# Kernel tuning notes

Measured on AMD Instinct MI355X. Metric: run time of the kernel, lower is better.

The kernel has to match this reference:

```python
import jax, jax.numpy as jnp
import numpy as np

N_NODES = 50000


def gat_layer(x, src, dst, W, att_s, att_d, b, concat):
    # PyG GATConv (eval mode): h = x W reshaped to [N, H, C]
    H, C = att_s.shape
    h = (x @ W).reshape(-1, H, C)                      # [N, H, C]
    a_s = (h * att_s).sum(-1)                          # [N, H]
    a_d = (h * att_d).sum(-1)                          # [N, H]
    e = jax.nn.leaky_relu(a_s[src] + a_d[dst], 0.2)    # [E, H]
    # scatter-softmax over destination nodes
    m = jax.ops.segment_max(e, dst, num_segments=N_NODES)
    alpha = jnp.exp(e - m[dst])
    denom = jax.ops.segment_sum(alpha, dst, num_segments=N_NODES)
    alpha = alpha / denom[dst]                         # [E, H]
    msg = h[src] * alpha[:, :, None]                   # [E, H, C]
    out = jax.ops.segment_sum(msg, dst, num_segments=N_NODES)  # [N, H, C]
    out = out.reshape(N_NODES, H * C) if concat else out.mean(axis=1)
    return out + b


def setup_inputs() -> dict:
    key = jax.random.key(0)
    ks = jax.random.split(key, 16)
    F_IN, HID, HEADS, NCLS, E = 512, 64, 4, 40, 800000
    x = jax.random.normal(ks[0], (N_NODES, F_IN), dtype=jnp.float32)
    edge_index = jax.random.randint(ks[1], (2, E), 0, N_NODES, dtype=jnp.int32)

    def glorot(k, shape):
        fan = shape[0]
        return jax.random.normal(k, shape, dtype=jnp.float32) / np.sqrt(fan)

    d1 = HID * HEADS  # 256
    return {
        "x": x,
        "edge_index": edge_index,
        "W1": glorot(ks[2], (F_IN, d1)),
        "as1": glorot(ks[3], (HEADS, HID)),
        "ad1": glorot(ks[4], (HEADS, HID)),
        "b1": jnp.zeros((d1,), jnp.float32),
        "W2": glorot(ks[5], (d1, d1)),
        "as2": glorot(ks[6], (HEADS, HID)),
        "ad2": glorot(ks[7], (HEADS, HID)),
        "b2": jnp.zeros((d1,), jnp.float32),
        "W3": glorot(ks[8], (d1, NCLS)),
        "as3": glorot(ks[9], (1, NCLS)),
        "ad3": glorot(ks[10], (1, NCLS)),
        "b3": jnp.zeros((NCLS,), jnp.float32),
    }


def reference(x, edge_index, W1, as1, ad1, b1, W2, as2, ad2, b2, W3, as3, ad3, b3):
    # add self-loops (PyG GATConv default)
    loops = jnp.arange(N_NODES, dtype=edge_index.dtype)
    src = jnp.concatenate([edge_index[0], loops])
    dst = jnp.concatenate([edge_index[1], loops])
    h = jax.nn.elu(gat_layer(x, src, dst, W1, as1, ad1, b1, True))
    h = jax.nn.elu(gat_layer(h, src, dst, W2, as2, ad2, b2, True))
    out = gat_layer(h, src, dst, W3, as3, ad3, b3, False)
    return out
```

## Files before the change

### kernel.cpp

```cpp
#include <hip/hip_runtime.h>
#include <stdint.h>

#define NN 50000
#define NB 196

typedef unsigned short u16;
typedef _Float16 f16;
typedef __attribute__((ext_vector_type(8))) _Float16 half8;
typedef __attribute__((ext_vector_type(4))) _Float16 half4;
typedef __attribute__((ext_vector_type(4))) float f32x4;

__device__ __forceinline__ void gload_lds16(const void* gsrc, void* ldst){
  __builtin_amdgcn_global_load_lds(
      (const __attribute__((address_space(1))) unsigned int*)gsrc,
      (__attribute__((address_space(3))) unsigned int*)ldst,
      16, 0, 0);
}

#define VMW(N)  asm volatile("s_waitcnt vmcnt(" #N ")" ::: "memory")
#define LGKM0() asm volatile("s_waitcnt lgkmcnt(0)" ::: "memory")
#define BARR()  asm volatile("s_barrier" ::: "memory")


__global__ void count_k(const int* __restrict__ dst, int* __restrict__ cnt, int E){
  int i = blockIdx.x * 256 + threadIdx.x;
  int tot = E + NN;
  if (i >= tot) return;
  int d = (i < E) ? dst[i] : (i - E);
  atomicAdd(&cnt[d], 1);
}

__global__ __launch_bounds__(256) void scan_part_k(const int* __restrict__ cnt,
                                                   int* __restrict__ bsum){
  __shared__ int lds[256];
  int tid = threadIdx.x;
  int idx = blockIdx.x * 256 + tid;
  lds[tid] = (idx < NN) ? cnt[idx] : 0;
  __syncthreads();
#pragma unroll
  for (int off = 128; off >= 1; off >>= 1){
    if (tid < off) lds[tid] += lds[tid + off];
    __syncthreads();
  }
  if (tid == 0) bsum[blockIdx.x] = lds[0];
}

__global__ __launch_bounds__(256) void scan_top_k(const int* __restrict__ bsum,
                                                  int* __restrict__ boff,
                                                  int* __restrict__ row_ptr){
  __shared__ int lds[256];
  int tid = threadIdx.x;
  int v = (tid < NB) ? bsum[tid] : 0;
  lds[tid] = v;
  __syncthreads();
#pragma unroll
  for (int off = 1; off < 256; off <<= 1){
    int t = (tid >= off) ? lds[tid - off] : 0;
    __syncthreads();
    lds[tid] += t;
    __syncthreads();
  }
  if (tid < NB) boff[tid] = lds[tid] - v;
  if (tid == 255) row_ptr[NN] = lds[255];
}

__global__ __launch_bounds__(256) void scan_fin_k(const int* __restrict__ cnt,
                                                  const int* __restrict__ boff,
                                                  int* __restrict__ row_ptr,
                                                  int* __restrict__ cursor){
  __shared__ int lds[256];
  int tid = threadIdx.x;
  int idx = blockIdx.x * 256 + tid;
  int v = (idx < NN) ? cnt[idx] : 0;
  lds[tid] = v;
  __syncthreads();
#pragma unroll
  for (int off = 1; off < 256; off <<= 1){
    int t = (tid >= off) ? lds[tid - off] : 0;
    __syncthreads();
    lds[tid] += t;
    __syncthreads();
  }
  if (idx < NN){
    int r = boff[blockIdx.x] + lds[tid] - v;
    row_ptr[idx] = r;
    cursor[idx]  = r;
  }
}

__global__ void scatter_k(const int* __restrict__ src, const int* __restrict__ dst,
                          int* __restrict__ cursor, int* __restrict__ csr, int E){
  int i = blockIdx.x * 256 + threadIdx.x;
  int tot = E + NN;
  if (i >= tot) return;
  int s, d;
  if (i < E){ s = src[i]; d = dst[i]; } else { s = i - E; d = i - E; }
  int pos = atomicAdd(&cursor[d], 1);
  csr[pos] = s;
}


__global__ void transpose_k(const float* __restrict__ W, f16* __restrict__ Wt, int K, int N){
  int i = blockIdx.x * 256 + threadIdx.x;
  if (i >= K * N) return;
  int n = i / K, k = i - n * K;
  Wt[i] = (f16)W[k * N + n];
}


template<bool A_FP32>
__global__ __launch_bounds__(512) void gemm_ring_k(const void* __restrict__ Aptr,
                                                   const f16* __restrict__ Bt,
                                                   f16* __restrict__ C,
                                                   const float* __restrict__ atts,
                                                   const float* __restrict__ attd,
                                                   float* __restrict__ a_s,
                                                   float* __restrict__ a_d,
                                                   int M, int K){
  constexpr int ABYTES = A_FP32 ? 8192 : 4096;
  constexpr int STEPB  = ABYTES + 8192;
  __shared__ __attribute__((aligned(16))) char lds[4 * STEPB];

  const int tid  = threadIdx.x;
  const int wave = tid >> 6, lane = tid & 63;
  const int quad = lane >> 4, l16 = lane & 15;
  const int wm = wave >> 1, wn = wave & 1;
  const int m0 = blockIdx.x * 64, n0 = blockIdx.y * 128;
  const int sc_l = lane >> 4, r_l = lane & 15;

  size_t bsrc = (size_t)(n0 + wave * 16 + r_l) * K + sc_l * 8;
  const int bdst = wave * 1024;
  size_t asrc; int adst; bool a_active = true;
  {
    int mt = wave & 3;
    int row = m0 + mt * 16 + r_l; if (row > M - 1) row = M - 1;
    if constexpr (A_FP32){
      int hp = wave >> 2;
      asrc = (size_t)row * K + sc_l * 8 + hp * 4;
      adst = hp * 4096 + mt * 1024;
    } else {
      asrc = (size_t)row * K + sc_l * 8;
      adst = mt * 1024;
      a_active = (wave < 4);
    }
  }
  const bool two_ops = A_FP32 ? true : (wave < 4);

  auto stage = [&](int buf, int k0){
    char* Ab = lds + buf * STEPB;
    char* Bb = Ab + ABYTES;
    if constexpr (A_FP32){
      gload_lds16((const float*)Aptr + asrc + k0, Ab + adst);
    } else {
      if (a_active) gload_lds16((const f16*)Aptr + asrc + k0, Ab + adst);
    }
    gload_lds16(Bt + bsrc + k0, Bb + bdst);
  };

  f32x4 acc[4] = {};

  auto compute = [&](int buf){
    char* Ab = lds + buf * STEPB;
    char* Bb = Ab + ABYTES;
    half8 af;
    if constexpr (A_FP32){
      const f32x4 lo = *(const f32x4*)(Ab + (wm * 64 + lane) * 16);
      const f32x4 hi = *(const f32x4*)(Ab + 4096 + (wm * 64 + lane) * 16);
      af[0] = (f16)lo.x; af[1] = (f16)lo.y; af[2] = (f16)lo.z; af[3] = (f16)lo.w;
      af[4] = (f16)hi.x; af[5] = (f16)hi.y; af[6] = (f16)hi.z; af[7] = (f16)hi.w;
    } else {
      af = *(const half8*)(Ab + (wm * 64 + lane) * 16);
    }
    half8 bf[4];
#pragma unroll
    for (int j = 0; j < 4; ++j)
      bf[j] = *(const half8*)(Bb + ((wn * 4 + j) * 64 + lane) * 16);
#pragma unroll
    for (int j = 0; j < 4; ++j)
      acc[j] = __builtin_amdgcn_mfma_f32_16x16x32_f16(af, bf[j], acc[j], 0, 0, 0);
  };

  stage(0, 0); stage(1, 32); stage(2, 64);

  const int nk = K >> 5;
  for (int t = 0; t < nk - 3; ++t){
    stage((t + 3) & 3, (t + 3) << 5);
    if (two_ops) VMW(6); else VMW(3);
    BARR();
    compute(t & 3);
    LGKM0();
    BARR();
  }
  if (two_ops) VMW(4); else VMW(2);
  BARR(); compute((nk - 3) & 3);
  if (two_ops) VMW(2); else VMW(1);
  BARR(); compute((nk - 2) & 3);
  VMW(0);
  BARR(); compute((nk - 1) & 3);

  const int N = 256;
  const int head = blockIdx.y * 2 + wn;
  float sA[4], dA[4];
#pragma unroll
  for (int j = 0; j < 4; ++j){
    sA[j] = atts[head * 64 + j * 16 + l16];
    dA[j] = attd[head * 64 + j * 16 + l16];
  }
#pragma unroll
  for (int r = 0; r < 4; ++r){
    int mm = m0 + wm * 16 + quad * 4 + r;
    float vs = 0.f, vd = 0.f;
#pragma unroll
    for (int j = 0; j < 4; ++j){
      float v = acc[j][r];
      vs += v * sA[j];
      vd += v * dA[j];
      int n = n0 + (wn * 4 + j) * 16 + l16;
      if (mm < M) C[(size_t)mm * N + n] = (f16)v;
    }
#pragma unroll
    for (int off = 8; off >= 1; off >>= 1){
      vs += __shfl_xor(vs, off);
      vd += __shfl_xor(vd, off);
    }
    if (l16 == 0 && mm < M){
      a_s[mm * 4 + head] = vs;
      a_d[mm * 4 + head] = vd;
    }
  }
}


__global__ __launch_bounds__(256) void gemm_n40_k(const f16* __restrict__ A,
                                                  const f16* __restrict__ Bt,
                                                  f16* __restrict__ C,
                                                  const float* __restrict__ atts,
                                                  const float* __restrict__ attd,
                                                  float* __restrict__ a_s,
                                                  float* __restrict__ a_d,
                                                  int M, int K){
  constexpr int ABYTES = 4096;
  constexpr int BBYTES = 3072;
  constexpr int STEPB  = ABYTES + BBYTES;
  __shared__ __attribute__((aligned(16))) char lds[4 * STEPB];

  const int tid  = threadIdx.x;
  const int wave = tid >> 6, lane = tid & 63;
  const int quad = lane >> 4, l16 = lane & 15;
  const int m0 = blockIdx.x * 64;
  const int sc_l = lane >> 4, r_l = lane & 15;

  int arow = m0 + wave * 16 + r_l; if (arow > M - 1) arow = M - 1;
  const size_t asrc = (size_t)arow * K + sc_l * 8;
  const int adst = wave * 1024;
  int brow = wave * 16 + r_l; if (brow > 39) brow = 39;
  const size_t bsrc = (size_t)brow * K + sc_l * 8;
  const int bdst = wave * 1024;
  const bool b_active = (wave < 3);
  const bool two_ops = b_active;

  auto stage = [&](int buf, int k0){
    char* Ab = lds + buf * STEPB;
    char* Bb = Ab + ABYTES;
    gload_lds16(A + asrc + k0, Ab + adst);
    if (b_active) gload_lds16(Bt + bsrc + k0, Bb + bdst);
  };

  f32x4 acc[3] = {};
  auto compute = [&](int buf){
    char* Ab = lds + buf * STEPB;
    char* Bb = Ab + ABYTES;
    half8 af = *(const half8*)(Ab + (wave * 64 + lane) * 16);
    half8 bf[3];
#pragma unroll
    for (int j = 0; j < 3; ++j)
      bf[j] = *(const half8*)(Bb + (j * 64 + lane) * 16);
#pragma unroll
    for (int j = 0; j < 3; ++j)
      acc[j] = __builtin_amdgcn_mfma_f32_16x16x32_f16(af, bf[j], acc[j], 0, 0, 0);
  };

  stage(0, 0); stage(1, 32); stage(2, 64);
  const int nk = K >> 5;
  for (int t = 0; t < nk - 3; ++t){
    stage((t + 3) & 3, (t + 3) << 5);
    if (two_ops) VMW(6); else VMW(3);
    BARR();
    compute(t & 3);
    LGKM0();
    BARR();
  }
  if (two_ops) VMW(4); else VMW(2);
  BARR(); compute((nk - 3) & 3);
  if (two_ops) VMW(2); else VMW(1);
  BARR(); compute((nk - 2) & 3);
  VMW(0);
  BARR(); compute((nk - 1) & 3);

  float sA[3], dA[3];
#pragma unroll
  for (int j = 0; j < 3; ++j){
    int n = j * 16 + l16;
    sA[j] = (n < 40) ? atts[n] : 0.f;
    dA[j] = (n < 40) ? attd[n] : 0.f;
  }
#pragma unroll
  for (int r = 0; r < 4; ++r){
    int mm = m0 + wave * 16 + quad * 4 + r;
    float vs = 0.f, vd = 0.f;
#pragma unroll
    for (int j = 0; j < 3; ++j){
      float v = acc[j][r];
      vs += v * sA[j];
      vd += v * dA[j];
      int n = j * 16 + l16;
      if (mm < M && n < 40) C[(size_t)mm * 40 + n] = (f16)v;
    }
#pragma unroll
    for (int off = 8; off >= 1; off >>= 1){
      vs += __shfl_xor(vs, off);
      vd += __shfl_xor(vd, off);
    }
    if (l16 == 0 && mm < M){
      a_s[mm] = vs;
      a_d[mm] = vd;
    }
  }
}


__device__ __forceinline__ float lrelu(float e){ return e > 0.f ? e : 0.2f * e; }

__global__ __launch_bounds__(256) void agg4_k(const f16* __restrict__ h,
                                              const float* __restrict__ a_s,
                                              const float* __restrict__ a_d,
                                              const int* __restrict__ row_ptr,
                                              const int* __restrict__ csr,
                                              const float* __restrict__ bias,
                                              f16* __restrict__ out){
  int w = blockIdx.x * 4 + (threadIdx.x >> 6);
  if (w >= NN) return;
  const int lane = threadIdx.x & 63;
  const int head = lane >> 4;
  const char* hb = (const char*)h;
  const uint32_t hoff_lane = (uint32_t)lane << 3;
  const float ad = a_d[w * 4 + head];
  const int beg = row_ptr[w], end = row_ptr[w + 1], endm1 = end - 1;

  float denom = 0.f, acc0 = 0.f, acc1 = 0.f, acc2 = 0.f, acc3 = 0.f;

  float ce[4]; half4 chv[4];
  float ne[4]; half4 nhv[4];

  auto ldgrp = [&](int base, float* EV, half4* HV){
#pragma unroll
    for (int q = 0; q < 4; ++q){
      int idx = base + q; idx = idx < endm1 ? idx : endm1;
      int s = csr[idx];
      EV[q] = a_s[(s << 2) + head];
      HV[q] = *(const half4*)(hb + (((uint32_t)s << 9) | hoff_lane));
    }
  };

  ldgrp(beg, ce, chv);
  int base = beg;
  while (true){
    bool more = base + 4 < end;
    if (more) ldgrp(base + 4, ne, nhv);
    int rem = end - base;
#pragma unroll
    for (int q = 0; q < 4; ++q){
      float al = __expf(lrelu(ce[q] + ad));
      al = (q < rem) ? al : 0.f;
      denom += al;
      acc0 += al * (float)chv[q].x;
      acc1 += al * (float)chv[q].y;
      acc2 += al * (float)chv[q].z;
      acc3 += al * (float)chv[q].w;
    }
    if (!more) break;
#pragma unroll
    for (int q = 0; q < 4; ++q){ ce[q] = ne[q]; chv[q] = nhv[q]; }
    base += 4;
  }

  float inv = 1.f / fmaxf(denom, 1e-30f);
  float o0 = acc0 * inv + bias[lane * 4 + 0];
  float o1 = acc1 * inv + bias[lane * 4 + 1];
  float o2 = acc2 * inv + bias[lane * 4 + 2];
  float o3 = acc3 * inv + bias[lane * 4 + 3];
  o0 = o0 > 0.f ? o0 : __expf(o0) - 1.f;
  o1 = o1 > 0.f ? o1 : __expf(o1) - 1.f;
  o2 = o2 > 0.f ? o2 : __expf(o2) - 1.f;
  o3 = o3 > 0.f ? o3 : __expf(o3) - 1.f;
  half4 rv; rv.x = (f16)o0; rv.y = (f16)o1; rv.z = (f16)o2; rv.w = (f16)o3;
  *(half4*)(out + (size_t)w * 256 + lane * 4) = rv;
}

__global__ __launch_bounds__(256) void agg1_k(const f16* __restrict__ h,
                                              const float* __restrict__ a_s,
                                              const float* __restrict__ a_d,
                                              const int* __restrict__ row_ptr,
                                              const int* __restrict__ csr,
                                              const float* __restrict__ bias,
                                              float* __restrict__ out){
  int w = blockIdx.x * 4 + (threadIdx.x >> 6);
  if (w >= NN) return;
  const int lane = threadIdx.x & 63;
  const int cl = (lane < 40) ? lane : 0;
  const float ad = a_d[w];
  const int beg = row_ptr[w], end = row_ptr[w + 1], endm1 = end - 1;

  float denom = 0.f, acc = 0.f;
  float ce[4], chv[4];
  float ne[4], nhv[4];

  auto ldgrp = [&](int base, float* EV, float* HV){
#pragma unroll
    for (int q = 0; q < 4; ++q){
      int idx = base + q; idx = idx < endm1 ? idx : endm1;
      int s = csr[idx];
      EV[q] = a_s[s];
      HV[q] = (float)h[(size_t)s * 40 + cl];
    }
  };

  ldgrp(beg, ce, chv);
  int base = beg;
  while (true){
    bool more = base + 4 < end;
    if (more) ldgrp(base + 4, ne, nhv);
    int rem = end - base;
#pragma unroll
    for (int q = 0; q < 4; ++q){
      float al = __expf(lrelu(ce[q] + ad));
      al = (q < rem) ? al : 0.f;
      denom += al;
      acc += al * chv[q];
    }
    if (!more) break;
#pragma unroll
    for (int q = 0; q < 4; ++q){ ce[q] = ne[q]; chv[q] = nhv[q]; }
    base += 4;
  }

  if (lane < 40){
    float o = acc / fmaxf(denom, 1e-30f) + bias[lane];
    out[(size_t)w * 40 + lane] = o;
  }
}


extern "C" void kernel_launch(void* const* d_in, const int* in_sizes, int n_in,
                              void* d_out, int out_size, void* d_ws, size_t ws_size,
                              hipStream_t stream){
  const float* x   = (const float*)d_in[0];
  const int*   ei  = (const int*)d_in[1];
  const float* W1  = (const float*)d_in[2];
  const float* as1 = (const float*)d_in[3];
  const float* ad1 = (const float*)d_in[4];
  const float* b1  = (const float*)d_in[5];
  const float* W2  = (const float*)d_in[6];
  const float* as2 = (const float*)d_in[7];
  const float* ad2 = (const float*)d_in[8];
  const float* b2  = (const float*)d_in[9];
  const float* W3  = (const float*)d_in[10];
  const float* as3 = (const float*)d_in[11];
  const float* ad3 = (const float*)d_in[12];
  const float* b3  = (const float*)d_in[13];

  const int E = in_sizes[1] / 2;
  const int ETOT = E + NN;
  const int* src_arr = ei;
  const int* dst_arr = ei + E;

  char* ws = (char*)d_ws;
  size_t off = 0;
  auto alloc = [&](size_t bytes) -> void* {
    void* p = ws + off; off += (bytes + 255) & ~(size_t)255; return p;
  };
  int*   cnt     = (int*)  alloc((size_t)NN * 4);
  int*   row_ptr = (int*)  alloc((size_t)(NN + 1) * 4);
  int*   cursor  = (int*)  alloc((size_t)NN * 4);
  int*   csr     = (int*)  alloc((size_t)ETOT * 4);
  int*   bsum    = (int*)  alloc((size_t)256 * 4);
  int*   boff    = (int*)  alloc((size_t)256 * 4);
  f16*   W1t     = (f16*)  alloc((size_t)512 * 256 * 2);
  f16*   W2t     = (f16*)  alloc((size_t)256 * 256 * 2);
  f16*   W3t     = (f16*)  alloc((size_t)256 * 40 * 2);
  float* a_s     = (float*)alloc((size_t)NN * 4 * 4);
  float* a_d     = (float*)alloc((size_t)NN * 4 * 4);
  f16*   hbuf    = (f16*)  alloc((size_t)NN * 256 * 2);
  f16*   xbuf    = (f16*)  alloc((size_t)NN * 256 * 2);
  (void)ws_size; (void)n_in; (void)out_size;

  hipMemsetAsync(cnt, 0, (size_t)NN * 4, stream);
  int egrid = (ETOT + 255) / 256;
  count_k    <<<egrid, 256, 0, stream>>>(dst_arr, cnt, E);
  scan_part_k<<<NB, 256, 0, stream>>>(cnt, bsum);
  scan_top_k <<<1, 256, 0, stream>>>(bsum, boff, row_ptr);
  scan_fin_k <<<NB, 256, 0, stream>>>(cnt, boff, row_ptr, cursor);
  scatter_k  <<<egrid, 256, 0, stream>>>(src_arr, dst_arr, cursor, csr, E);

  transpose_k<<<(512 * 256 + 255) / 256, 256, 0, stream>>>(W1, W1t, 512, 256);
  transpose_k<<<(256 * 256 + 255) / 256, 256, 0, stream>>>(W2, W2t, 256, 256);
  transpose_k<<<(256 * 40  + 255) / 256, 256, 0, stream>>>(W3, W3t, 256, 40);

  dim3 blk512(512);
  dim3 blk(256);
  dim3 gT((NN + 63) / 64, 2);
  dim3 gC((NN + 63) / 64, 1);
  int nodeblocks = (NN + 3) / 4;

  gemm_ring_k<true> <<<gT, blk512, 0, stream>>>(x, W1t, hbuf, as1, ad1, a_s, a_d, NN, 512);
  agg4_k<<<nodeblocks, blk, 0, stream>>>(hbuf, a_s, a_d, row_ptr, csr, b1, xbuf);

  gemm_ring_k<false><<<gT, blk512, 0, stream>>>(xbuf, W2t, hbuf, as2, ad2, a_s, a_d, NN, 256);
  agg4_k<<<nodeblocks, blk, 0, stream>>>(hbuf, a_s, a_d, row_ptr, csr, b2, xbuf);

  gemm_n40_k<<<gC, blk, 0, stream>>>(xbuf, W3t, hbuf, as3, ad3, a_s, a_d, NN, 256);
  agg1_k<<<nodeblocks, blk, 0, stream>>>(hbuf, a_s, a_d, row_ptr, csr, b3, (float*)d_out);
}
```

Before: 534.3 us.

## Enlarge GEMM tile to 128x256 with 4x4 MFMA per wave

The layer-1/2 GEMM now gives each block a 128-row by full 256-column tile instead of 64x128. Each wave computes a 4x4 grid of 16x16 MFMA tiles, so every A and B fragment loaded from LDS is reused more and A is read from global memory only once per row block. The cost is a larger LDS ring (up to 128KB for the fp32-A case), 64 accumulator vectors per thread, and fewer blocks, which can lower occupancy and latency hiding.

```diff
diff --git a/kernel.cpp b/kernel.cpp
--- a/kernel.cpp
+++ b/kernel.cpp
@@ -109,75 +109,79 @@
 
 
 template<bool A_FP32>
-__global__ __launch_bounds__(512) void gemm_ring_k(const void* __restrict__ Aptr,
-                                                   const f16* __restrict__ Bt,
-                                                   f16* __restrict__ C,
-                                                   const float* __restrict__ atts,
-                                                   const float* __restrict__ attd,
-                                                   float* __restrict__ a_s,
-                                                   float* __restrict__ a_d,
-                                                   int M, int K){
-  constexpr int ABYTES = A_FP32 ? 8192 : 4096;
-  constexpr int STEPB  = ABYTES + 8192;
+__global__ __launch_bounds__(512) void gemm_big_k(const void* __restrict__ Aptr,
+                                                  const f16* __restrict__ Bt,
+                                                  f16* __restrict__ C,
+                                                  const float* __restrict__ atts,
+                                                  const float* __restrict__ attd,
+                                                  float* __restrict__ a_s,
+                                                  float* __restrict__ a_d,
+                                                  int M, int K){
+  constexpr int ABYTES = A_FP32 ? 16384 : 8192;
+  constexpr int STEPB  = ABYTES + 16384;
   __shared__ __attribute__((aligned(16))) char lds[4 * STEPB];
 
   const int tid  = threadIdx.x;
   const int wave = tid >> 6, lane = tid & 63;
   const int quad = lane >> 4, l16 = lane & 15;
-  const int wm = wave >> 1, wn = wave & 1;
-  const int m0 = blockIdx.x * 64, n0 = blockIdx.y * 128;
+  const int wm = wave >> 2, wn = wave & 3;
+  const int m0 = blockIdx.x * 128;
   const int sc_l = lane >> 4, r_l = lane & 15;
 
-  size_t bsrc = (size_t)(n0 + wave * 16 + r_l) * K + sc_l * 8;
-  const int bdst = wave * 1024;
-  size_t asrc; int adst; bool a_active = true;
-  {
-    int mt = wave & 3;
-    int row = m0 + mt * 16 + r_l; if (row > M - 1) row = M - 1;
-    if constexpr (A_FP32){
-      int hp = wave >> 2;
-      asrc = (size_t)row * K + sc_l * 8 + hp * 4;
-      adst = hp * 4096 + mt * 1024;
-    } else {
-      asrc = (size_t)row * K + sc_l * 8;
-      adst = mt * 1024;
-      a_active = (wave < 4);
-    }
-  }
-  const bool two_ops = A_FP32 ? true : (wave < 4);
+  const size_t bsrc0 = (size_t)(wave * 16 + r_l) * K + sc_l * 8;
+  const size_t bsrc1 = (size_t)((wave + 8) * 16 + r_l) * K + sc_l * 8;
+  const int bdst0 = wave * 1024;
+  const int bdst1 = (wave + 8) * 1024;
+
+  int arow = m0 + wave * 16 + r_l; if (arow > M - 1) arow = M - 1;
+  const size_t asrc0 = (size_t)arow * K + sc_l * 8;
+  const size_t asrc1 = asrc0 + 4;
+  const int adst0 = wave * 1024;
+  const int adst1 = 8192 + wave * 1024;
 
   auto stage = [&](int buf, int k0){
     char* Ab = lds + buf * STEPB;
     char* Bb = Ab + ABYTES;
     if constexpr (A_FP32){
-      gload_lds16((const float*)Aptr + asrc + k0, Ab + adst);
+      const float* A = (const float*)Aptr;
+      gload_lds16(A + asrc0 + k0, Ab + adst0);
+      gload_lds16(A + asrc1 + k0, Ab + adst1);
     } else {
-      if (a_active) gload_lds16((const f16*)Aptr + asrc + k0, Ab + adst);
-    }
-    gload_lds16(Bt + bsrc + k0, Bb + bdst);
-  };
-
-  f32x4 acc[4] = {};
+      gload_lds16((const f16*)Aptr + asrc0 + k0, Ab + adst0);
+    }
+    gload_lds16(Bt + bsrc0 + k0, Bb + bdst0);
+    gload_lds16(Bt + bsrc1 + k0, Bb + bdst1);
+  };
+
+  f32x4 acc[4][4] = {};
 
   auto compute = [&](int buf){
     char* Ab = lds + buf * STEPB;
     char* Bb = Ab + ABYTES;
-    half8 af;
+    half8 af[4], bf[4];
     if constexpr (A_FP32){
-      const f32x4 lo = *(const f32x4*)(Ab + (wm * 64 + lane) * 16);
-      const f32x4 hi = *(const f32x4*)(Ab + 4096 + (wm * 64 + lane) * 16);
-      af[0] = (f16)lo.x; af[1] = (f16)lo.y; af[2] = (f16)lo.z; af[3] = (f16)lo.w;
-      af[4] = (f16)hi.x; af[5] = (f16)hi.y; af[6] = (f16)hi.z; af[7] = (f16)hi.w;
+#pragma unroll
+      for (int i = 0; i < 4; ++i){
+        const f32x4 lo = *(const f32x4*)(Ab + ((wm * 4 + i) * 64 + lane) * 16);
+        const f32x4 hi = *(const f32x4*)(Ab + 8192 + ((wm * 4 + i) * 64 + lane) * 16);
+        half8 v;
+        v[0] = (f16)lo.x; v[1] = (f16)lo.y; v[2] = (f16)lo.z; v[3] = (f16)lo.w;
+        v[4] = (f16)hi.x; v[5] = (f16)hi.y; v[6] = (f16)hi.z; v[7] = (f16)hi.w;
+        af[i] = v;
+      }
     } else {
-      af = *(const half8*)(Ab + (wm * 64 + lane) * 16);
-    }
-    half8 bf[4];
+#pragma unroll
+      for (int i = 0; i < 4; ++i)
+        af[i] = *(const half8*)(Ab + ((wm * 4 + i) * 64 + lane) * 16);
+    }
 #pragma unroll
     for (int j = 0; j < 4; ++j)
       bf[j] = *(const half8*)(Bb + ((wn * 4 + j) * 64 + lane) * 16);
 #pragma unroll
-    for (int j = 0; j < 4; ++j)
-      acc[j] = __builtin_amdgcn_mfma_f32_16x16x32_f16(af, bf[j], acc[j], 0, 0, 0);
+    for (int i = 0; i < 4; ++i)
+#pragma unroll
+      for (int j = 0; j < 4; ++j)
+        acc[i][j] = __builtin_amdgcn_mfma_f32_16x16x32_f16(af[i], bf[j], acc[i][j], 0, 0, 0);
   };
 
   stage(0, 0); stage(1, 32); stage(2, 64);
@@ -185,21 +189,21 @@
   const int nk = K >> 5;
   for (int t = 0; t < nk - 3; ++t){
     stage((t + 3) & 3, (t + 3) << 5);
-    if (two_ops) VMW(6); else VMW(3);
+    if constexpr (A_FP32) VMW(12); else VMW(9);
     BARR();
     compute(t & 3);
     LGKM0();
     BARR();
   }
-  if (two_ops) VMW(4); else VMW(2);
+  if constexpr (A_FP32) VMW(8); else VMW(6);
   BARR(); compute((nk - 3) & 3);
-  if (two_ops) VMW(2); else VMW(1);
+  if constexpr (A_FP32) VMW(4); else VMW(3);
   BARR(); compute((nk - 2) & 3);
   VMW(0);
   BARR(); compute((nk - 1) & 3);
 
   const int N = 256;
-  const int head = blockIdx.y * 2 + wn;
+  const int head = wn;
   float sA[4], dA[4];
 #pragma unroll
   for (int j = 0; j < 4; ++j){
@@ -207,25 +211,28 @@
     dA[j] = attd[head * 64 + j * 16 + l16];
   }
 #pragma unroll
-  for (int r = 0; r < 4; ++r){
-    int mm = m0 + wm * 16 + quad * 4 + r;
-    float vs = 0.f, vd = 0.f;
-#pragma unroll
-    for (int j = 0; j < 4; ++j){
-      float v = acc[j][r];
-      vs += v * sA[j];
-      vd += v * dA[j];
-      int n = n0 + (wn * 4 + j) * 16 + l16;
-      if (mm < M) C[(size_t)mm * N + n] = (f16)v;
-    }
-#pragma unroll
-    for (int off = 8; off >= 1; off >>= 1){
-      vs += __shfl_xor(vs, off);
-      vd += __shfl_xor(vd, off);
-    }
-    if (l16 == 0 && mm < M){
-      a_s[mm * 4 + head] = vs;
-      a_d[mm * 4 + head] = vd;
+  for (int i = 0; i < 4; ++i){
+#pragma unroll
+    for (int r = 0; r < 4; ++r){
+      int mm = m0 + wm * 64 + i * 16 + quad * 4 + r;
+      float vs = 0.f, vd = 0.f;
+#pragma unroll
+      for (int j = 0; j < 4; ++j){
+        float v = acc[i][j][r];
+        vs += v * sA[j];
+        vd += v * dA[j];
+        int n = wn * 64 + j * 16 + l16;
+        if (mm < M) C[(size_t)mm * N + n] = (f16)v;
+      }
+#pragma unroll
+      for (int off = 8; off >= 1; off >>= 1){
+        vs += __shfl_xor(vs, off);
+        vd += __shfl_xor(vd, off);
+      }
+      if (l16 == 0 && mm < M){
+        a_s[mm * 4 + head] = vs;
+        a_d[mm * 4 + head] = vd;
+      }
     }
   }
 }
@@ -508,14 +515,14 @@
 
   dim3 blk512(512);
   dim3 blk(256);
-  dim3 gT((NN + 63) / 64, 2);
-  dim3 gC((NN + 63) / 64, 1);
+  dim3 gB((NN + 127) / 128);
+  dim3 gC((NN + 63) / 64);
   int nodeblocks = (NN + 3) / 4;
 
-  gemm_ring_k<true> <<<gT, blk512, 0, stream>>>(x, W1t, hbuf, as1, ad1, a_s, a_d, NN, 512);
+  gemm_big_k<true> <<<gB, blk512, 0, stream>>>(x, W1t, hbuf, as1, ad1, a_s, a_d, NN, 512);
   agg4_k<<<nodeblocks, blk, 0, stream>>>(hbuf, a_s, a_d, row_ptr, csr, b1, xbuf);
 
-  gemm_ring_k<false><<<gT, blk512, 0, stream>>>(xbuf, W2t, hbuf, as2, ad2, a_s, a_d, NN, 256);
+  gemm_big_k<false><<<gB, blk512, 0, stream>>>(xbuf, W2t, hbuf, as2, ad2, a_s, a_d, NN, 256);
   agg4_k<<<nodeblocks, blk, 0, stream>>>(hbuf, a_s, a_d, row_ptr, csr, b2, xbuf);
 
   gemm_n40_k<<<gC, blk, 0, stream>>>(xbuf, W3t, hbuf, as3, ad3, a_s, a_d, NN, 256);
```

After: 518.8 us. 2.9% less time.
